# Kernel tuning notes

Measured on AMD Instinct MI355X. Metric: run time of the kernel, lower is better.

The kernel has to match this reference:

```python
import jax, jax.numpy as jnp
import numpy as np

N = 50000   # nodes
E = 800000  # edges
D = 64      # dim_node
H = 64      # hidden_channels
G = 512     # graphs in batch


def setup_inputs() -> dict:
    key = jax.random.key(0)
    ks = jax.random.split(key, 13)
    s = 0.05
    return dict(
        x=jax.random.normal(ks[0], (N, D), jnp.float32),
        edge_index=jax.random.randint(ks[1], (2, E), 0, N, dtype=jnp.int32),
        batch_idx=jnp.sort(jax.random.randint(ks[2], (N,), 0, G, dtype=jnp.int32)),
        W0=jax.random.normal(ks[3], (D, H), jnp.float32) * s,
        b0=jnp.zeros((H,), jnp.float32),
        W1=jax.random.normal(ks[4], (H, H), jnp.float32) * s,
        b1=jnp.zeros((H,), jnp.float32),
        W2=jax.random.normal(ks[5], (H, H), jnp.float32) * s,
        b2=jnp.zeros((H,), jnp.float32),
        lin1_w=jax.random.normal(ks[6], (H, H), jnp.float32) * s,
        lin1_b=jnp.zeros((H,), jnp.float32),
        lin2_w=jax.random.normal(ks[7], (H, 1), jnp.float32) * s,
        lin2_b=jnp.zeros((1,), jnp.float32),
    )


def gcn_conv(x, W, b, src, dst, n):
    """PyG GCNConv: out = D^{-1/2} (A + I) D^{-1/2} X W + b (self-loops added)."""
    h = x @ W                                   # [n, H] transform first (cheaper)
    loop = jnp.arange(n, dtype=src.dtype)
    row = jnp.concatenate([src, loop])          # message sources (incl. self-loops)
    col = jnp.concatenate([dst, loop])          # aggregation targets
    deg = jax.ops.segment_sum(jnp.ones_like(col, jnp.float32), col, num_segments=n)
    dinv = jnp.where(deg > 0, jax.lax.rsqrt(deg), 0.0)
    norm = dinv[row] * dinv[col]                # [E+n]
    msg = h[row] * norm[:, None]                # gather + scale
    return jax.ops.segment_sum(msg, col, num_segments=n) + b


def reference(x, edge_index, batch_idx, W0, b0, W1, b1, W2, b2,
              lin1_w, lin1_b, lin2_w, lin2_b):
    src, dst = edge_index[0], edge_index[1]
    h = jax.nn.relu(gcn_conv(x, W0, b0, src, dst, N))   # dropout(p=0, eval) = identity
    h = jax.nn.relu(gcn_conv(h, W1, b1, src, dst, N))
    h = jax.nn.relu(gcn_conv(h, W2, b2, src, dst, N))
    # global_mean_pool over graph ids
    sums = jax.ops.segment_sum(h, batch_idx, num_segments=G)            # [G, H]
    cnt = jax.ops.segment_sum(jnp.ones((N,), jnp.float32), batch_idx, num_segments=G)
    pooled = sums / jnp.maximum(cnt, 1.0)[:, None]
    h = jax.nn.relu(pooled @ lin1_w + lin1_b)
    return h @ lin2_w + lin2_b                                          # [G, 1]
```

## Files before the change

### kernel.cpp

```cpp
#include <hip/hip_runtime.h>
#include <math.h>

#define NN 50000
#define EE 800000
#define HH 64
#define GG 512
#define SCAN_NB ((NN + 1023) / 1024)

typedef unsigned short ushort_t;
typedef unsigned int uint_t;

__device__ __forceinline__ ushort_t f32_to_bf16(float f) {
    uint_t u = __float_as_uint(f);
    uint_t bias = 0x7FFFu + ((u >> 16) & 1u);
    return (ushort_t)((u + bias) >> 16);
}
__device__ __forceinline__ float bf16_to_f32(ushort_t h) {
    return __uint_as_float(((uint_t)h) << 16);
}


__global__ void k_deg(const int* __restrict__ dst, int* __restrict__ deg,
                      int* __restrict__ rank) {
    int e = blockIdx.x * blockDim.x + threadIdx.x;
    if (e < EE) rank[e] = atomicAdd(&deg[dst[e]], 1);
}


__global__ void __launch_bounds__(1024) k_scan1(const int* __restrict__ deg,
                                                int* __restrict__ rowptr,
                                                int* __restrict__ bsum,
                                                float* __restrict__ dinv) {
    int tid = threadIdx.x;
    int lane = tid & 63, w = tid >> 6;
    int i = blockIdx.x * 1024 + tid;
    int v = (i < NN) ? deg[i] : 0;
    if (i < NN)       dinv[i] = 1.0f / sqrtf((float)(v + 1));
    else if (i == NN) dinv[i] = 0.0f;
    int x = v;
#pragma unroll
    for (int off = 1; off < 64; off <<= 1) {
        int y = __shfl_up(x, off);
        if (lane >= off) x += y;
    }
    __shared__ int ws[16];
    if (lane == 63) ws[w] = x;
    __syncthreads();
    if (tid < 16) {
        int y = ws[tid];
        int z = y;
#pragma unroll
        for (int off = 1; off < 16; off <<= 1) {
            int t2 = __shfl_up(z, off);
            if (tid >= off) z += t2;
        }
        ws[tid] = z - y;
    }
    __syncthreads();
    int excl = x - v + ws[w];
    if (i <= NN) rowptr[i] = excl;
    if (tid == 1023) bsum[blockIdx.x] = excl + v;
}

__global__ void __launch_bounds__(64) k_scan2(int* __restrict__ bsum) {
    int lane = threadIdx.x;
    int v = (lane < SCAN_NB) ? bsum[lane] : 0;
    int x = v;
#pragma unroll
    for (int off = 1; off < 64; off <<= 1) {
        int y = __shfl_up(x, off);
        if (lane >= off) x += y;
    }
    if (lane < SCAN_NB) bsum[lane] = x - v;
}


__global__ void k_fill(const int* __restrict__ src, const int* __restrict__ dst,
                       const int* __restrict__ rank,
                       const int* __restrict__ rowptr, const int* __restrict__ bsum,
                       const int* __restrict__ batch,
                       int* __restrict__ csr_src, int* __restrict__ cnt) {
    int tid = blockIdx.x * blockDim.x + threadIdx.x;
    if (tid < EE) {
        int d = dst[tid];
        csr_src[rowptr[d] + bsum[d >> 10] + rank[tid]] = src[tid];
    } else if (tid < EE + NN) {
        atomicAdd(&cnt[batch[tid - EE]], 1);
    }
}


template<bool RELU>
__global__ void __launch_bounds__(256) k_xform(const float* __restrict__ x,
                                               const float* __restrict__ W,
                                               const float* __restrict__ dinv,
                                               ushort_t* __restrict__ t) {
    __shared__ float sW[64 * 64];
    __shared__ float sX[32 * 65];
    int tid = threadIdx.x;
    for (int k = tid; k < 64 * 64; k += 256) sW[k] = W[k];
    int row0 = blockIdx.x * 32;
    for (int v = tid; v < 32 * 16; v += 256) {
        int r  = v >> 4;
        int k4 = (v & 15) * 4;
        int row = row0 + r;
        float4 val = make_float4(0.f, 0.f, 0.f, 0.f);
        if (row < NN) val = *(const float4*)(x + (size_t)row * 64 + k4);
        if (RELU) {
            val.x = fmaxf(val.x, 0.f); val.y = fmaxf(val.y, 0.f);
            val.z = fmaxf(val.z, 0.f); val.w = fmaxf(val.w, 0.f);
        }
        sX[r * 65 + k4 + 0] = val.x;
        sX[r * 65 + k4 + 1] = val.y;
        sX[r * 65 + k4 + 2] = val.z;
        sX[r * 65 + k4 + 3] = val.w;
    }
    __syncthreads();
    int r  = tid >> 3;
    int c0 = (tid & 7) * 8;
    float acc[8] = {0.f, 0.f, 0.f, 0.f, 0.f, 0.f, 0.f, 0.f};
    for (int k = 0; k < 64; ++k) {
        float xv = sX[r * 65 + k];
#pragma unroll
        for (int j = 0; j < 8; ++j) acc[j] = fmaf(xv, sW[k * 64 + c0 + j], acc[j]);
    }
    int row = row0 + r;
    if (row <= NN) {
        float dv = dinv[row];
        uint_t pk[4];
#pragma unroll
        for (int j = 0; j < 4; ++j) {
            ushort_t lo = f32_to_bf16(acc[2 * j] * dv);
            ushort_t hi = f32_to_bf16(acc[2 * j + 1] * dv);
            pk[j] = (uint_t)lo | ((uint_t)hi << 16);
        }
        uint4* o = (uint4*)(t + (size_t)row * 64 + c0);
        *o = make_uint4(pk[0], pk[1], pk[2], pk[3]);
    }
}


template<bool POOL>
__global__ void __launch_bounds__(256) k_gather(const ushort_t* __restrict__ t,
                                                const float* __restrict__ dinv,
                                                const int* __restrict__ rowptr,
                                                const int* __restrict__ bsum,
                                                const int* __restrict__ csr_src,
                                                const float* __restrict__ b,
                                                const int* __restrict__ batch,
                                                float* __restrict__ out) {
    int i = __builtin_amdgcn_readfirstlane((blockIdx.x * blockDim.x + threadIdx.x) >> 6);
    int c = threadIdx.x & 63;
    if (i >= NN) return;
    int e   = __builtin_amdgcn_readfirstlane(rowptr[i]     + bsum[i >> 10]);
    int end = __builtin_amdgcn_readfirstlane(rowptr[i + 1] + bsum[(i + 1) >> 10]);
    float acc = bf16_to_f32(t[(size_t)i * 64 + c]);
    float a0 = 0.f, a1 = 0.f, a2 = 0.f, a3 = 0.f;
    for (; e < end; e += 16) {
        int s[16];
#pragma unroll
        for (int j = 0; j < 16; ++j) {
            int sj = csr_src[e + j];
            s[j] = (e + j < end) ? sj : NN;
        }
        ushort_t v[16];
#pragma unroll
        for (int j = 0; j < 16; ++j) v[j] = t[(size_t)s[j] * 64 + c];
#pragma unroll
        for (int j = 0; j < 16; ++j) {
            float f = bf16_to_f32(v[j]);
            if ((j & 3) == 0)      a0 += f;
            else if ((j & 3) == 1) a1 += f;
            else if ((j & 3) == 2) a2 += f;
            else                   a3 += f;
        }
    }
    acc += (a0 + a1) + (a2 + a3);
    float r = fmaf(acc, dinv[i], b[c]);
    if (POOL) {
        atomicAdd(&out[(size_t)batch[i] * 64 + c], fmaxf(r, 0.0f));
    } else {
        out[(size_t)i * 64 + c] = r;
    }
}


__global__ void __launch_bounds__(64) k_head(const float* __restrict__ pooled,
                                             const int* __restrict__ cnt,
                                             const float* __restrict__ w1,
                                             const float* __restrict__ b1,
                                             const float* __restrict__ w2,
                                             const float* __restrict__ b2,
                                             float* __restrict__ out) {
    int g = blockIdx.x;
    int c = threadIdx.x;
    __shared__ float sp[64];
    float cf = fmaxf((float)cnt[g], 1.0f);
    sp[c] = pooled[(size_t)g * 64 + c] / cf;
    __syncthreads();
    float acc = b1[c];
    for (int k = 0; k < 64; ++k) acc = fmaf(sp[k], w1[k * 64 + c], acc);
    float h1 = fmaxf(acc, 0.0f);
    float p = h1 * w2[c];
#pragma unroll
    for (int off = 32; off > 0; off >>= 1) p += __shfl_down(p, off);
    if (c == 0) out[g] = p + b2[0];
}


extern "C" void kernel_launch(void* const* d_in, const int* in_sizes, int n_in,
                              void* d_out, int out_size, void* d_ws, size_t ws_size,
                              hipStream_t stream) {
    const float* x      = (const float*)d_in[0];
    const int*   ei     = (const int*)d_in[1];
    const int*   batch  = (const int*)d_in[2];
    const float* W0     = (const float*)d_in[3];
    const float* b0     = (const float*)d_in[4];
    const float* W1     = (const float*)d_in[5];
    const float* b1     = (const float*)d_in[6];
    const float* W2     = (const float*)d_in[7];
    const float* b2     = (const float*)d_in[8];
    const float* lin1w  = (const float*)d_in[9];
    const float* lin1b  = (const float*)d_in[10];
    const float* lin2w  = (const float*)d_in[11];
    const float* lin2b  = (const float*)d_in[12];
    float* out = (float*)d_out;

    const int* src = ei;
    const int* dst = ei + EE;

    char* ws = (char*)d_ws;
    size_t off = 0;
    auto carve = [&](size_t bytes) {
        void* p = ws + off;
        off = (off + bytes + 255) & ~(size_t)255;
        return p;
    };
    int*      deg      = (int*)carve((size_t)NN * 4);
    float*    pooled   = (float*)carve((size_t)GG * 64 * 4);
    int*      cnt      = (int*)carve((size_t)GG * 4);
    size_t zero_span = off;
    float*    dinv     = (float*)carve((size_t)(NN + 1) * 4);
    int*      rowptr   = (int*)carve((size_t)(NN + 1) * 4);
    int*      bsum     = (int*)carve((size_t)SCAN_NB * 4);
    int*      rank     = (int*)carve((size_t)EE * 4);
    int*      csr_src  = (int*)carve((size_t)(EE + 16) * 4);
    ushort_t* bufT     = (ushort_t*)carve((size_t)(NN + 1) * 64 * 2);
    float*    bufA     = (float*)carve((size_t)NN * 64 * 4);

    hipMemsetAsync(deg, 0, zero_span, stream);

    k_deg  <<<(EE + 255) / 256, 256, 0, stream>>>(dst, deg, rank);
    k_scan1<<<SCAN_NB, 1024, 0, stream>>>(deg, rowptr, bsum, dinv);
    k_scan2<<<1, 64, 0, stream>>>(bsum);
    k_fill <<<(EE + NN + 255) / 256, 256, 0, stream>>>(src, dst, rank, rowptr,
                                                       bsum, batch, csr_src, cnt);

    const int xgrid = (NN + 1 + 31) / 32;
    const int ggrid = (NN * 64) / 256;

    k_xform<false><<<xgrid, 256, 0, stream>>>(x, W0, dinv, bufT);
    k_gather<false><<<ggrid, 256, 0, stream>>>(bufT, dinv, rowptr, bsum, csr_src,
                                               b0, batch, bufA);
    k_xform<true><<<xgrid, 256, 0, stream>>>(bufA, W1, dinv, bufT);
    k_gather<false><<<ggrid, 256, 0, stream>>>(bufT, dinv, rowptr, bsum, csr_src,
                                               b1, batch, bufA);
    k_xform<true><<<xgrid, 256, 0, stream>>>(bufA, W2, dinv, bufT);
    k_gather<true><<<ggrid, 256, 0, stream>>>(bufT, dinv, rowptr, bsum, csr_src,
                                              b2, batch, pooled);

    k_head<<<GG, 64, 0, stream>>>(pooled, cnt, lin1w, lin1b, lin2w, lin2b, out);
}
```

Before: 309.6 us.

## Build CSR with node-range partitioned LDS histograms instead of global atomics

Replaces the global-atomic degree count and rank-based scatter with 32 workgroups, each owning one node range. Each workgroup scans every edge, counting and placing only the edges that land in its range, using LDS atomics. This removes the global atomic traffic and the rank array, at the cost of each of the 32 blocks reading all edges. Only 32 workgroups run, so much of the GPU sits idle. The per-graph count moves to a separate small kernel.

```diff
diff --git a/kernel.cpp b/kernel.cpp
--- a/kernel.cpp
+++ b/kernel.cpp
@@ -6,6 +6,8 @@
 #define HH 64
 #define GG 512
 #define SCAN_NB ((NN + 1023) / 1024)
+#define FW_NWG 32
+#define FW_CHUNK ((NN + FW_NWG - 1) / FW_NWG)
 
 typedef unsigned short ushort_t;
 typedef unsigned int uint_t;
@@ -20,10 +22,28 @@
 }
 
 
-__global__ void k_deg(const int* __restrict__ dst, int* __restrict__ deg,
-                      int* __restrict__ rank) {
-    int e = blockIdx.x * blockDim.x + threadIdx.x;
-    if (e < EE) rank[e] = atomicAdd(&deg[dst[e]], 1);
+__global__ void __launch_bounds__(1024) k_count(const int* __restrict__ dst,
+                                                int* __restrict__ deg) {
+    __shared__ int cnt[FW_CHUNK];
+    int tid = threadIdx.x;
+    int lo = blockIdx.x * FW_CHUNK;
+    int hi = min(lo + FW_CHUNK, NN);
+    for (int j = tid; j < FW_CHUNK; j += 1024) cnt[j] = 0;
+    __syncthreads();
+    for (int e0 = tid * 8; e0 < EE; e0 += 8192) {
+        int4 a = *(const int4*)(dst + e0);
+        int4 b = *(const int4*)(dst + e0 + 4);
+        if (a.x >= lo && a.x < hi) atomicAdd(&cnt[a.x - lo], 1);
+        if (a.y >= lo && a.y < hi) atomicAdd(&cnt[a.y - lo], 1);
+        if (a.z >= lo && a.z < hi) atomicAdd(&cnt[a.z - lo], 1);
+        if (a.w >= lo && a.w < hi) atomicAdd(&cnt[a.w - lo], 1);
+        if (b.x >= lo && b.x < hi) atomicAdd(&cnt[b.x - lo], 1);
+        if (b.y >= lo && b.y < hi) atomicAdd(&cnt[b.y - lo], 1);
+        if (b.z >= lo && b.z < hi) atomicAdd(&cnt[b.z - lo], 1);
+        if (b.w >= lo && b.w < hi) atomicAdd(&cnt[b.w - lo], 1);
+    }
+    __syncthreads();
+    for (int j = tid; lo + j < hi; j += 1024) deg[lo + j] = cnt[j];
 }
 
 
@@ -75,18 +95,42 @@
 }
 
 
-__global__ void k_fill(const int* __restrict__ src, const int* __restrict__ dst,
-                       const int* __restrict__ rank,
-                       const int* __restrict__ rowptr, const int* __restrict__ bsum,
-                       const int* __restrict__ batch,
-                       int* __restrict__ csr_src, int* __restrict__ cnt) {
-    int tid = blockIdx.x * blockDim.x + threadIdx.x;
-    if (tid < EE) {
-        int d = dst[tid];
-        csr_src[rowptr[d] + bsum[d >> 10] + rank[tid]] = src[tid];
-    } else if (tid < EE + NN) {
-        atomicAdd(&cnt[batch[tid - EE]], 1);
-    }
+__global__ void __launch_bounds__(1024) k_fillp(const int* __restrict__ src,
+                                                const int* __restrict__ dst,
+                                                const int* __restrict__ rowptr,
+                                                const int* __restrict__ bsum,
+                                                int* __restrict__ csr_src) {
+    __shared__ int cur[FW_CHUNK];
+    __shared__ int base[FW_CHUNK];
+    int tid = threadIdx.x;
+    int lo = blockIdx.x * FW_CHUNK;
+    int hi = min(lo + FW_CHUNK, NN);
+    for (int j = tid; j < FW_CHUNK; j += 1024) {
+        cur[j] = 0;
+        int i = lo + j;
+        base[j] = (i < NN) ? rowptr[i] + bsum[i >> 10] : 0;
+    }
+    __syncthreads();
+    for (int e0 = tid * 8; e0 < EE; e0 += 8192) {
+        int4 da = *(const int4*)(dst + e0);
+        int4 db = *(const int4*)(dst + e0 + 4);
+        int4 sa = *(const int4*)(src + e0);
+        int4 sb = *(const int4*)(src + e0 + 4);
+        if (da.x >= lo && da.x < hi) { int p = atomicAdd(&cur[da.x - lo], 1); csr_src[base[da.x - lo] + p] = sa.x; }
+        if (da.y >= lo && da.y < hi) { int p = atomicAdd(&cur[da.y - lo], 1); csr_src[base[da.y - lo] + p] = sa.y; }
+        if (da.z >= lo && da.z < hi) { int p = atomicAdd(&cur[da.z - lo], 1); csr_src[base[da.z - lo] + p] = sa.z; }
+        if (da.w >= lo && da.w < hi) { int p = atomicAdd(&cur[da.w - lo], 1); csr_src[base[da.w - lo] + p] = sa.w; }
+        if (db.x >= lo && db.x < hi) { int p = atomicAdd(&cur[db.x - lo], 1); csr_src[base[db.x - lo] + p] = sb.x; }
+        if (db.y >= lo && db.y < hi) { int p = atomicAdd(&cur[db.y - lo], 1); csr_src[base[db.y - lo] + p] = sb.y; }
+        if (db.z >= lo && db.z < hi) { int p = atomicAdd(&cur[db.z - lo], 1); csr_src[base[db.z - lo] + p] = sb.z; }
+        if (db.w >= lo && db.w < hi) { int p = atomicAdd(&cur[db.w - lo], 1); csr_src[base[db.w - lo] + p] = sb.w; }
+    }
+}
+
+
+__global__ void k_cnt(const int* __restrict__ batch, int* __restrict__ cnt) {
+    int i = blockIdx.x * blockDim.x + threadIdx.x;
+    if (i < NN) atomicAdd(&cnt[batch[i]], 1);
 }
 
 
@@ -130,9 +174,9 @@
         uint_t pk[4];
 #pragma unroll
         for (int j = 0; j < 4; ++j) {
-            ushort_t lo = f32_to_bf16(acc[2 * j] * dv);
-            ushort_t hi = f32_to_bf16(acc[2 * j + 1] * dv);
-            pk[j] = (uint_t)lo | ((uint_t)hi << 16);
+            ushort_t lol = f32_to_bf16(acc[2 * j] * dv);
+            ushort_t hih = f32_to_bf16(acc[2 * j + 1] * dv);
+            pk[j] = (uint_t)lol | ((uint_t)hih << 16);
         }
         uint4* o = (uint4*)(t + (size_t)row * 64 + c0);
         *o = make_uint4(pk[0], pk[1], pk[2], pk[3]);
@@ -236,25 +280,24 @@
         off = (off + bytes + 255) & ~(size_t)255;
         return p;
     };
-    int*      deg      = (int*)carve((size_t)NN * 4);
     float*    pooled   = (float*)carve((size_t)GG * 64 * 4);
     int*      cnt      = (int*)carve((size_t)GG * 4);
     size_t zero_span = off;
+    int*      deg      = (int*)carve((size_t)NN * 4);
     float*    dinv     = (float*)carve((size_t)(NN + 1) * 4);
     int*      rowptr   = (int*)carve((size_t)(NN + 1) * 4);
     int*      bsum     = (int*)carve((size_t)SCAN_NB * 4);
-    int*      rank     = (int*)carve((size_t)EE * 4);
     int*      csr_src  = (int*)carve((size_t)(EE + 16) * 4);
     ushort_t* bufT     = (ushort_t*)carve((size_t)(NN + 1) * 64 * 2);
     float*    bufA     = (float*)carve((size_t)NN * 64 * 4);
 
-    hipMemsetAsync(deg, 0, zero_span, stream);
-
-    k_deg  <<<(EE + 255) / 256, 256, 0, stream>>>(dst, deg, rank);
+    hipMemsetAsync(pooled, 0, zero_span, stream);
+
+    k_count<<<FW_NWG, 1024, 0, stream>>>(dst, deg);
     k_scan1<<<SCAN_NB, 1024, 0, stream>>>(deg, rowptr, bsum, dinv);
     k_scan2<<<1, 64, 0, stream>>>(bsum);
-    k_fill <<<(EE + NN + 255) / 256, 256, 0, stream>>>(src, dst, rank, rowptr,
-                                                       bsum, batch, csr_src, cnt);
+    k_fillp<<<FW_NWG, 1024, 0, stream>>>(src, dst, rowptr, bsum, csr_src);
+    k_cnt  <<<(NN + 255) / 256, 256, 0, stream>>>(batch, cnt);
 
     const int xgrid = (NN + 1 + 31) / 32;
     const int ggrid = (NN * 64) / 256;
```

After: 469.6 us. 51.7% more time.
